# Optimization experiments

Measured on AMD Instinct MI355X. Metric: run time of the kernel, lower is better.

Reference implementation:

```python
import jax, jax.numpy as jnp
import numpy as np

N_NODES = 50000
N_EDGES = 800000
F_IN = 128
HIDDEN = 32
HEADS = 4
F_OUT = 64
NEG_SLOPE = 0.2


def setup_inputs() -> dict:
    key = jax.random.key(0)
    ks = jax.random.split(key, 9)
    x = jax.random.normal(ks[0], (N_NODES, F_IN), dtype=jnp.float32)
    edge_index = jax.random.randint(ks[1], (2, N_EDGES), 0, N_NODES, dtype=jnp.int64)
    edge_weight = jax.random.uniform(ks[2], (N_EDGES,), dtype=jnp.float32)
    # GATConv parameters
    W = jax.random.normal(ks[3], (F_IN, HEADS * HIDDEN), dtype=jnp.float32) * (1.0 / np.sqrt(F_IN))
    a_src = jax.random.normal(ks[4], (HEADS, HIDDEN), dtype=jnp.float32) * 0.1
    a_dst = jax.random.normal(ks[5], (HEADS, HIDDEN), dtype=jnp.float32) * 0.1
    bias = jnp.zeros((HEADS * HIDDEN,), dtype=jnp.float32)
    # output linear
    W2 = jax.random.normal(ks[6], (HEADS * HIDDEN, F_OUT), dtype=jnp.float32) * (1.0 / np.sqrt(HEADS * HIDDEN))
    b2 = jnp.zeros((F_OUT,), dtype=jnp.float32)
    return {"x": x, "edge_index": edge_index, "edge_weight": edge_weight,
            "W": W, "a_src": a_src, "a_dst": a_dst, "bias": bias,
            "W2": W2, "b2": b2}


def reference(x, edge_index, edge_weight, W, a_src, a_dst, bias, W2, b2):
    src, dst = edge_index[0], edge_index[1]
    # linear transform per head: [N, H, C]
    h = (x @ W).reshape(-1, HEADS, HIDDEN)
    # per-node attention logits: [N, H]
    alpha_s = jnp.einsum('nhc,hc->nh', h, a_src)
    alpha_d = jnp.einsum('nhc,hc->nh', h, a_dst)
    # per-edge scores: [E, H]
    e = alpha_s[src] + alpha_d[dst]
    e = jnp.where(e >= 0, e, NEG_SLOPE * e)  # LeakyReLU(0.2)
    # segment softmax over destination neighborhoods
    m = jax.ops.segment_max(e, dst, num_segments=N_NODES)  # [N, H]
    ex = jnp.exp(e - m[dst])
    denom = jax.ops.segment_sum(ex, dst, num_segments=N_NODES)  # [N, H]
    alpha = ex / (denom[dst] + 1e-16)  # [E, H]
    # weighted scatter-add aggregation: [N, H, C]
    msgs = alpha[:, :, None] * h[src]
    out = jax.ops.segment_sum(msgs, dst, num_segments=N_NODES)
    out = out.reshape(-1, HEADS * HIDDEN) + bias
    out = jax.nn.elu(out)
    return out @ W2 + b2
```

## Files before the change

### kernel.cpp

```cpp
#include <hip/hip_runtime.h>

#define N_NODES 50000
#define N_EDGES 800000
#define F_IN 128
#define HH 128
#define HEADS 4
#define HIDDEN 32
#define F_OUT 64
#define NEG_SLOPE 0.2f
#define CAP 64

#define NODE_BLOCKS ((N_NODES + 31) / 32)
#define FILL_BLOCKS ((N_EDGES / 4 + 255) / 256)

typedef __attribute__((ext_vector_type(8))) short short8v;
typedef __attribute__((ext_vector_type(4))) float float4v;

__device__ __forceinline__ unsigned short f2bf(float f) {
    unsigned int u = __float_as_uint(f);
    u = (u + 0x7FFFu + ((u >> 16) & 1u)) >> 16;
    return (unsigned short)u;
}

__global__ __launch_bounds__(256) void k_prep(
    const float* __restrict__ W, const float* __restrict__ a_src,
    const float* __restrict__ a_dst,
    unsigned short* __restrict__ Wf, unsigned short* __restrict__ Waf)
{
    const int b = blockIdx.x;
    const int t = threadIdx.x;

    if (b < 8) {
        const int ks = b >> 1, nn = b & 1;
        const int w = t >> 6, lane = t & 63, l15 = lane & 15, l4 = lane >> 4;
        const int c  = w * 32 + nn * 16 + l15;
        const int kb = ks * 32 + l4 * 8;
        short8v frag;
        #pragma unroll
        for (int j = 0; j < 8; ++j)
            frag[j] = (short)f2bf(W[(size_t)(kb + j) * HH + c]);
        *(short8v*)&Wf[(size_t)((ks * 2 + nn) * 256 + t) * 8] = frag;
        return;
    }

    __shared__ float Wa[F_IN][8];
    #pragma unroll
    for (int i = 0; i < 4; ++i) {
        int idx = t * 4 + i;
        int k = idx >> 3, col = idx & 7;
        const float* av = (col < 4) ? a_src : a_dst;
        int hd = col & 3;
        float s = 0.f;
        #pragma unroll
        for (int cc = 0; cc < 32; ++cc)
            s = fmaf(W[(size_t)k * HH + hd * 32 + cc], av[hd * 32 + cc], s);
        Wa[k][col] = s;
    }
    __syncthreads();

    if (t < 64) {
        const int l15 = t & 15, l4 = t >> 4;
        #pragma unroll
        for (int ks = 0; ks < 4; ++ks) {
            short8v frag;
            #pragma unroll
            for (int j = 0; j < 8; ++j)
                frag[j] = (l15 < 8) ? (short)f2bf(Wa[ks * 32 + l4 * 8 + j][l15]) : (short)0;
            *(short8v*)&Waf[(size_t)(ks * 64 + t) * 8] = frag;
        }
    }
}

__global__ __launch_bounds__(256) void k_node_fill(
    const float* __restrict__ x,
    const unsigned short* __restrict__ Wf, const unsigned short* __restrict__ Waf,
    unsigned short* __restrict__ h_bf,
    float* __restrict__ as_out, float* __restrict__ ad_out,
    const int* __restrict__ ei, int* __restrict__ cursor, int* __restrict__ bucket)
{
    __shared__ __align__(16) unsigned short xs[32][136];

    if (blockIdx.x >= NODE_BLOCKS) {
        int e0 = ((blockIdx.x - NODE_BLOCKS) * 256 + threadIdx.x) * 4;
        if (e0 < N_EDGES) {
            int4 s4 = *(const int4*)&ei[e0];
            int4 d4 = *(const int4*)&ei[N_EDGES + e0];
            bucket[(size_t)d4.x * CAP + (atomicAdd(&cursor[d4.x], 1) & (CAP - 1))] = s4.x;
            bucket[(size_t)d4.y * CAP + (atomicAdd(&cursor[d4.y], 1) & (CAP - 1))] = s4.y;
            bucket[(size_t)d4.z * CAP + (atomicAdd(&cursor[d4.z], 1) & (CAP - 1))] = s4.z;
            bucket[(size_t)d4.w * CAP + (atomicAdd(&cursor[d4.w], 1) & (CAP - 1))] = s4.w;
        }
        return;
    }

    const int tid  = threadIdx.x;
    const int base = blockIdx.x * 32;

    for (int i = tid; i < 32 * 32; i += 256) {
        int r = i >> 5, c4 = i & 31;
        int n = base + r;
        float4 v = (n < N_NODES) ? *(const float4*)&x[(size_t)n * F_IN + c4 * 4]
                                 : make_float4(0.f, 0.f, 0.f, 0.f);
        ushort4 hv;
        hv.x = f2bf(v.x); hv.y = f2bf(v.y); hv.z = f2bf(v.z); hv.w = f2bf(v.w);
        *(ushort4*)&xs[r][c4 * 4] = hv;
    }
    __syncthreads();

    const int w    = tid >> 6;
    const int lane = tid & 63;
    const int l15  = lane & 15;
    const int l4   = lane >> 4;

    short8v bfrag[4][2], wafrag[4];
    #pragma unroll
    for (int ks = 0; ks < 4; ++ks) {
        bfrag[ks][0] = *(const short8v*)&Wf[(size_t)((ks * 2 + 0) * 256 + tid) * 8];
        bfrag[ks][1] = *(const short8v*)&Wf[(size_t)((ks * 2 + 1) * 256 + tid) * 8];
        wafrag[ks]   = *(const short8v*)&Waf[(size_t)(ks * 64 + lane) * 8];
    }

    float4v acc[2][2] = {};
    float4v accL[2] = {};
    #pragma unroll
    for (int ks = 0; ks < 4; ++ks) {
        short8v a0 = *(const short8v*)&xs[l15][ks * 32 + l4 * 8];
        short8v a1 = *(const short8v*)&xs[16 + l15][ks * 32 + l4 * 8];
        acc[0][0] = __builtin_amdgcn_mfma_f32_16x16x32_bf16(a0, bfrag[ks][0], acc[0][0], 0, 0, 0);
        acc[0][1] = __builtin_amdgcn_mfma_f32_16x16x32_bf16(a0, bfrag[ks][1], acc[0][1], 0, 0, 0);
        acc[1][0] = __builtin_amdgcn_mfma_f32_16x16x32_bf16(a1, bfrag[ks][0], acc[1][0], 0, 0, 0);
        acc[1][1] = __builtin_amdgcn_mfma_f32_16x16x32_bf16(a1, bfrag[ks][1], acc[1][1], 0, 0, 0);
        accL[0]   = __builtin_amdgcn_mfma_f32_16x16x32_bf16(a0, wafrag[ks], accL[0], 0, 0, 0);
        accL[1]   = __builtin_amdgcn_mfma_f32_16x16x32_bf16(a1, wafrag[ks], accL[1], 0, 0, 0);
    }

    #pragma unroll
    for (int m = 0; m < 2; ++m) {
        #pragma unroll
        for (int reg = 0; reg < 4; ++reg) {
            int node = base + m * 16 + l4 * 4 + reg;
            if (node >= N_NODES) continue;
            h_bf[(size_t)node * HH + w * 32 + l15]      = f2bf(acc[m][0][reg]);
            h_bf[(size_t)node * HH + w * 32 + 16 + l15] = f2bf(acc[m][1][reg]);
            if (w == 0 && l15 < 8) {
                float lg = accL[m][reg];
                if (l15 < 4) as_out[node * HEADS + l15]       = lg;
                else         ad_out[node * HEADS + (l15 - 4)] = lg;
            }
        }
    }
}

__global__ __launch_bounds__(256) void k_gather(
    const int* __restrict__ cnt_arr, const int* __restrict__ bucket,
    const float* __restrict__ as_, const float* __restrict__ ad_,
    const unsigned short* __restrict__ h_bf, float* __restrict__ agg)
{
    int gid = blockIdx.x * 256 + threadIdx.x;
    int n = gid >> 6;
    if (n >= N_NODES) return;
    const int lane = gid & 63;
    const int hd  = lane >> 4;
    const int e16 = lane & 15;

    const float advv = ad_[n * 4 + hd];
    const int cnt = cnt_arr[n];
    const int* brow = &bucket[(size_t)n * CAP];

    float accx = 0.f, accy = 0.f, sum = 0.f;

    for (int cb = 0; cb < cnt; cb += 16) {
        int m = cnt - cb; if (m > 16) m = 16;
        int s = 0; float exown = 0.f;
        if (e16 < m) {
            s = brow[cb + e16];
            float lg = as_[s * 4 + hd] + advv;
            lg = lg >= 0.f ? lg : NEG_SLOPE * lg;
            exown = __expf(lg);
        }

#define GAT_BODY(j)                                                            \
        {                                                                      \
            float al = __shfl(exown, (hd << 4) + (j));                         \
            int   sj = __shfl(s,     (hd << 4) + (j));                         \
            unsigned int hv = *(const unsigned int*)&h_bf[(size_t)sj * HH + lane * 2]; \
            sum += al;                                                         \
            accx = fmaf(al, __uint_as_float((hv & 0xFFFFu) << 16), accx);      \
            accy = fmaf(al, __uint_as_float(hv & 0xFFFF0000u), accy);          \
        }

        if (m == 16) {
            #pragma unroll
            for (int j = 0; j < 16; ++j) GAT_BODY(j)
        } else {
            for (int j = 0; j < m; ++j) GAT_BODY(j)
        }
#undef GAT_BODY
    }

    float inv = 1.f / (sum + 1e-16f);
    *(float2*)&agg[(size_t)n * HH + lane * 2] = make_float2(accx * inv, accy * inv);
}

__global__ __launch_bounds__(256) void k_output(
    const float* __restrict__ agg, const float* __restrict__ bias,
    const float* __restrict__ W2, const float* __restrict__ b2,
    float* __restrict__ out)
{
    __shared__ float eb[64][132];

    const int tid  = threadIdx.x;
    const int base = blockIdx.x * 64;

    for (int i = tid; i < 64 * 32; i += 256) {
        int r = i >> 5, c4 = i & 31;
        int n = base + r;
        float4 v = (n < N_NODES) ? *(const float4*)&agg[(size_t)n * HH + c4 * 4]
                                 : make_float4(0.f, 0.f, 0.f, 0.f);
        float4 b = *(const float4*)&bias[c4 * 4];
        v.x += b.x; v.y += b.y; v.z += b.z; v.w += b.w;
        v.x = v.x > 0.f ? v.x : __expf(v.x) - 1.f;
        v.y = v.y > 0.f ? v.y : __expf(v.y) - 1.f;
        v.z = v.z > 0.f ? v.z : __expf(v.z) - 1.f;
        v.w = v.w > 0.f ? v.w : __expf(v.w) - 1.f;
        *(float4*)&eb[r][c4 * 4] = v;
    }
    __syncthreads();

    const int cg = tid & 15;
    const int q  = tid >> 4;

    float4 b2v = *(const float4*)&b2[cg * 4];
    float4 acc[4] = { b2v, b2v, b2v, b2v };
    for (int k4 = 0; k4 < 32; ++k4) {
        const float* wr = &W2[(k4 * 4) * F_OUT + cg * 4];
        float4 w0 = *(const float4*)(wr);
        float4 w1 = *(const float4*)(wr + F_OUT);
        float4 w2 = *(const float4*)(wr + 2 * F_OUT);
        float4 w3 = *(const float4*)(wr + 3 * F_OUT);
        #pragma unroll
        for (int j = 0; j < 4; ++j) {
            float4 xv = *(const float4*)&eb[q * 4 + j][k4 * 4];
            acc[j].x = fmaf(xv.x, w0.x, acc[j].x); acc[j].y = fmaf(xv.x, w0.y, acc[j].y);
            acc[j].z = fmaf(xv.x, w0.z, acc[j].z); acc[j].w = fmaf(xv.x, w0.w, acc[j].w);
            acc[j].x = fmaf(xv.y, w1.x, acc[j].x); acc[j].y = fmaf(xv.y, w1.y, acc[j].y);
            acc[j].z = fmaf(xv.y, w1.z, acc[j].z); acc[j].w = fmaf(xv.y, w1.w, acc[j].w);
            acc[j].x = fmaf(xv.z, w2.x, acc[j].x); acc[j].y = fmaf(xv.z, w2.y, acc[j].y);
            acc[j].z = fmaf(xv.z, w2.z, acc[j].z); acc[j].w = fmaf(xv.z, w2.w, acc[j].w);
            acc[j].x = fmaf(xv.w, w3.x, acc[j].x); acc[j].y = fmaf(xv.w, w3.y, acc[j].y);
            acc[j].z = fmaf(xv.w, w3.z, acc[j].z); acc[j].w = fmaf(xv.w, w3.w, acc[j].w);
        }
    }
    #pragma unroll
    for (int j = 0; j < 4; ++j) {
        int n = base + q * 4 + j;
        if (n < N_NODES)
            *(float4*)&out[(size_t)n * F_OUT + cg * 4] = acc[j];
    }
}

extern "C" void kernel_launch(void* const* d_in, const int* in_sizes, int n_in,
                              void* d_out, int out_size, void* d_ws, size_t ws_size,
                              hipStream_t stream)
{
    const float* x     = (const float*)d_in[0];
    const int*   ei    = (const int*)  d_in[1];
    const float* W     = (const float*)d_in[3];
    const float* a_src = (const float*)d_in[4];
    const float* a_dst = (const float*)d_in[5];
    const float* bias  = (const float*)d_in[6];
    const float* W2    = (const float*)d_in[7];
    const float* b2    = (const float*)d_in[8];
    float* out = (float*)d_out;

    char* ws = (char*)d_ws;
    unsigned short* Wf   = (unsigned short*)ws;
    unsigned short* Waf  = Wf + 8 * 256 * 8;
    unsigned short* h_bf = Waf + 4 * 64 * 8;
    float* as_   = (float*)(h_bf + (size_t)N_NODES * HH);
    float* ad_   = as_ + (size_t)N_NODES * HEADS;
    int*   cursor= (int*)(ad_ + (size_t)N_NODES * HEADS);
    int*   bucket= cursor + N_NODES;
    float* agg   = (float*)(bucket + (size_t)N_NODES * CAP);

    hipMemsetAsync(cursor, 0, (size_t)N_NODES * sizeof(int), stream);

    k_prep<<<9, 256, 0, stream>>>(W, a_src, a_dst, Wf, Waf);
    k_node_fill<<<NODE_BLOCKS + FILL_BLOCKS, 256, 0, stream>>>(
        x, Wf, Waf, h_bf, as_, ad_, ei, cursor, bucket);
    k_gather<<<(N_NODES * 64 + 255) / 256, 256, 0, stream>>>(cursor, bucket, as_, ad_, h_bf, agg);
    k_output<<<(N_NODES + 63) / 64, 256, 0, stream>>>(agg, bias, W2, b2, out);
}
```

Baseline: 133.5 us.

## Fold cursor zeroing into prep, stage h stores via LDS, store aggregate as bf16

Replaces the separate memset of the cursor array with extra blocks in the prep kernel, removing one launch. The node-transform kernel now stages the bf16 results in shared memory and writes them as 16-byte rows instead of scattered 2-byte stores. The gather kernel writes the aggregated features as bf16 rather than fp32, which halves that intermediate's traffic into the output kernel. The cost is extra precision loss on the aggregate and two added block barriers.

```diff
diff --git a/kernel.cpp b/kernel.cpp
--- a/kernel.cpp
+++ b/kernel.cpp
@@ -12,6 +12,7 @@
 
 #define NODE_BLOCKS ((N_NODES + 31) / 32)
 #define FILL_BLOCKS ((N_EDGES / 4 + 255) / 256)
+#define ZERO_BLOCKS ((N_NODES + 255) / 256)
 
 typedef __attribute__((ext_vector_type(8))) short short8v;
 typedef __attribute__((ext_vector_type(4))) float float4v;
@@ -21,14 +22,24 @@
     u = (u + 0x7FFFu + ((u >> 16) & 1u)) >> 16;
     return (unsigned short)u;
 }
+__device__ __forceinline__ float bf2f(unsigned short s) {
+    return __uint_as_float((unsigned int)s << 16);
+}
 
 __global__ __launch_bounds__(256) void k_prep(
     const float* __restrict__ W, const float* __restrict__ a_src,
     const float* __restrict__ a_dst,
-    unsigned short* __restrict__ Wf, unsigned short* __restrict__ Waf)
+    unsigned short* __restrict__ Wf, unsigned short* __restrict__ Waf,
+    int* __restrict__ cursor)
 {
     const int b = blockIdx.x;
     const int t = threadIdx.x;
+
+    if (b >= 9) {
+        int i = (b - 9) * 256 + t;
+        if (i < N_NODES) cursor[i] = 0;
+        return;
+    }
 
     if (b < 8) {
         const int ks = b >> 1, nn = b & 1;
@@ -134,27 +145,43 @@
         accL[1]   = __builtin_amdgcn_mfma_f32_16x16x32_bf16(a1, wafrag[ks], accL[1], 0, 0, 0);
     }
 
-    #pragma unroll
-    for (int m = 0; m < 2; ++m) {
-        #pragma unroll
-        for (int reg = 0; reg < 4; ++reg) {
-            int node = base + m * 16 + l4 * 4 + reg;
-            if (node >= N_NODES) continue;
-            h_bf[(size_t)node * HH + w * 32 + l15]      = f2bf(acc[m][0][reg]);
-            h_bf[(size_t)node * HH + w * 32 + 16 + l15] = f2bf(acc[m][1][reg]);
-            if (w == 0 && l15 < 8) {
+    if (w == 0 && l15 < 8) {
+        #pragma unroll
+        for (int m = 0; m < 2; ++m) {
+            #pragma unroll
+            for (int reg = 0; reg < 4; ++reg) {
+                int node = base + m * 16 + l4 * 4 + reg;
+                if (node >= N_NODES) continue;
                 float lg = accL[m][reg];
                 if (l15 < 4) as_out[node * HEADS + l15]       = lg;
                 else         ad_out[node * HEADS + (l15 - 4)] = lg;
             }
         }
     }
+
+    __syncthreads();
+    #pragma unroll
+    for (int m = 0; m < 2; ++m) {
+        #pragma unroll
+        for (int reg = 0; reg < 4; ++reg) {
+            int r = m * 16 + l4 * 4 + reg;
+            xs[r][w * 32 + l15]      = f2bf(acc[m][0][reg]);
+            xs[r][w * 32 + 16 + l15] = f2bf(acc[m][1][reg]);
+        }
+    }
+    __syncthreads();
+    for (int i = tid; i < 32 * 16; i += 256) {
+        int r = i >> 4, c8 = i & 15;
+        int n = base + r;
+        if (n < N_NODES)
+            *(short8v*)&h_bf[(size_t)n * HH + c8 * 8] = *(const short8v*)&xs[r][c8 * 8];
+    }
 }
 
 __global__ __launch_bounds__(256) void k_gather(
     const int* __restrict__ cnt_arr, const int* __restrict__ bucket,
     const float* __restrict__ as_, const float* __restrict__ ad_,
-    const unsigned short* __restrict__ h_bf, float* __restrict__ agg)
+    const unsigned short* __restrict__ h_bf, unsigned short* __restrict__ agg_bf)
 {
     int gid = blockIdx.x * 256 + threadIdx.x;
     int n = gid >> 6;
@@ -199,11 +226,13 @@
     }
 
     float inv = 1.f / (sum + 1e-16f);
-    *(float2*)&agg[(size_t)n * HH + lane * 2] = make_float2(accx * inv, accy * inv);
+    unsigned int packed = (unsigned int)f2bf(accx * inv)
+                        | ((unsigned int)f2bf(accy * inv) << 16);
+    *(unsigned int*)&agg_bf[(size_t)n * HH + lane * 2] = packed;
 }
 
 __global__ __launch_bounds__(256) void k_output(
-    const float* __restrict__ agg, const float* __restrict__ bias,
+    const unsigned short* __restrict__ agg_bf, const float* __restrict__ bias,
     const float* __restrict__ W2, const float* __restrict__ b2,
     float* __restrict__ out)
 {
@@ -212,18 +241,24 @@
     const int tid  = threadIdx.x;
     const int base = blockIdx.x * 64;
 
-    for (int i = tid; i < 64 * 32; i += 256) {
-        int r = i >> 5, c4 = i & 31;
+    for (int i = tid; i < 64 * 16; i += 256) {
+        int r = i >> 4, c8 = i & 15;
         int n = base + r;
-        float4 v = (n < N_NODES) ? *(const float4*)&agg[(size_t)n * HH + c4 * 4]
-                                 : make_float4(0.f, 0.f, 0.f, 0.f);
-        float4 b = *(const float4*)&bias[c4 * 4];
-        v.x += b.x; v.y += b.y; v.z += b.z; v.w += b.w;
-        v.x = v.x > 0.f ? v.x : __expf(v.x) - 1.f;
-        v.y = v.y > 0.f ? v.y : __expf(v.y) - 1.f;
-        v.z = v.z > 0.f ? v.z : __expf(v.z) - 1.f;
-        v.w = v.w > 0.f ? v.w : __expf(v.w) - 1.f;
-        *(float4*)&eb[r][c4 * 4] = v;
+        float v[8];
+        if (n < N_NODES) {
+            ushort4 p0 = *(const ushort4*)&agg_bf[(size_t)n * HH + c8 * 8];
+            ushort4 p1 = *(const ushort4*)&agg_bf[(size_t)n * HH + c8 * 8 + 4];
+            v[0] = bf2f(p0.x); v[1] = bf2f(p0.y); v[2] = bf2f(p0.z); v[3] = bf2f(p0.w);
+            v[4] = bf2f(p1.x); v[5] = bf2f(p1.y); v[6] = bf2f(p1.z); v[7] = bf2f(p1.w);
+        } else {
+            #pragma unroll
+            for (int j = 0; j < 8; ++j) v[j] = 0.f;
+        }
+        #pragma unroll
+        for (int j = 0; j < 8; ++j) {
+            float t = v[j] + bias[c8 * 8 + j];
+            eb[r][c8 * 8 + j] = t > 0.f ? t : __expf(t) - 1.f;
+        }
     }
     __syncthreads();
 
@@ -281,13 +316,11 @@
     float* ad_   = as_ + (size_t)N_NODES * HEADS;
     int*   cursor= (int*)(ad_ + (size_t)N_NODES * HEADS);
     int*   bucket= cursor + N_NODES;
-    float* agg   = (float*)(bucket + (size_t)N_NODES * CAP);
-
-    hipMemsetAsync(cursor, 0, (size_t)N_NODES * sizeof(int), stream);
-
-    k_prep<<<9, 256, 0, stream>>>(W, a_src, a_dst, Wf, Waf);
+    unsigned short* agg_bf = (unsigned short*)(bucket + (size_t)N_NODES * CAP);
+
+    k_prep<<<9 + ZERO_BLOCKS, 256, 0, stream>>>(W, a_src, a_dst, Wf, Waf, cursor);
     k_node_fill<<<NODE_BLOCKS + FILL_BLOCKS, 256, 0, stream>>>(
         x, Wf, Waf, h_bf, as_, ad_, ei, cursor, bucket);
-    k_gather<<<(N_NODES * 64 + 255) / 256, 256, 0, stream>>>(cursor, bucket, as_, ad_, h_bf, agg);
-    k_output<<<(N_NODES + 63) / 64, 256, 0, stream>>>(agg, bias, W2, b2, out);
-}
+    k_gather<<<(N_NODES * 64 + 255) / 256, 256, 0, stream>>>(cursor, bucket, as_, ad_, h_bf, agg_bf);
+    k_output<<<(N_NODES + 63) / 64, 256, 0, stream>>>(agg_bf, bias, W2, b2, out);
+}
```

Result: faster. 124.9 us (-6.4%).
